# Kernel tuning notes

Hardware: AMD Instinct MI355X
Metric: run time of the kernel (lower is better)

The kernel has to match this reference:

```python
import jax, jax.numpy as jnp
import numpy as np

N, E, T = 10000, 160000, 1600000
D, C, H = 256, 64, 1024  # d_model, d_message/channels, 4*d_model ffn hidden


def setup_inputs() -> dict:
    key = jax.random.key(0)
    ks = jax.random.split(key, 20)
    rn = lambda k, s, sc=1.0: jax.random.normal(k, s, dtype=jnp.float32) * sc
    return {
        "x": rn(ks[0], (N, D)),
        "y": rn(ks[1], (E, D)),
        "r": rn(ks[2], (E, 3)),
        "src": jax.random.randint(ks[3], (E,), 0, N),
        "dst": jax.random.randint(ks[4], (E,), 0, N),
        "tsrc": jax.random.randint(ks[5], (T,), 0, E),
        "tdst": jax.random.randint(ks[6], (T,), 0, E),
        "W_src": rn(ks[7], (D, C), 0.05), "b_src": rn(ks[8], (C,), 0.05),
        "W_dst": rn(ks[9], (D, C), 0.05), "b_dst": rn(ks[10], (C,), 0.05),
        "W_edge": rn(ks[11], (D, C), 0.05), "b_edge": rn(ks[12], (C,), 0.05),
        "attn": rn(ks[13], (C,), 0.05),
        "W1": rn(ks[14], (C, H), 0.05), "b1": rn(ks[15], (H,), 0.05),
        "W2": rn(ks[16], (H, D), 0.05), "b2": rn(ks[17], (D,), 0.05),
    }


def reference(x, y, r, src, dst, tsrc, tdst,
              W_src, b_src, W_dst, b_dst, W_edge, b_edge,
              attn, W1, b1, W2, b2):
    # per-bond message: xij = Lin_src(x)[src] + Lin_dst(x)[dst] + Lin_edge(y)  -> (E, C)
    xij = (x @ W_src + b_src)[src] + (x @ W_dst + b_dst)[dst] + (y @ W_edge + b_edge)

    # triplet angle cosine via normalized (negated) bond vectors  -> (T,)
    rnorm = -r / jnp.linalg.norm(r, axis=1, keepdims=True)
    cos_jik = jnp.clip(jnp.sum(rnorm[tsrc] * rnorm[tdst], axis=-1), -1.0 + 1e-6, 1.0 - 1e-6)

    # Chebyshev expansion: T_n(cos) = cos(n * arccos(cos))  -> (T, C)
    n = jnp.arange(C, dtype=jnp.float32)
    z_jik = jnp.cos(n[None, :] * jnp.arccos(cos_jik)[:, None])

    # triplet feature and attention logit
    e_jik = jax.nn.silu(z_jik + xij[tsrc] + xij[tdst])          # (T, C)
    logits = e_jik @ attn                                        # (T,)

    # segment softmax over triplets grouped by destination bond (edge_softmax)
    mx = jax.ops.segment_max(logits, tdst, num_segments=E)
    ex = jnp.exp(logits - mx[tdst])
    den = jax.ops.segment_sum(ex, tdst, num_segments=E)
    a = ex / den[tdst]                                           # (T,)

    # attention-weighted scatter-sum of neighbor bond features  -> (E, C)
    ft = jax.ops.segment_sum(xij[tsrc] * a[:, None], tdst, num_segments=E)

    # feedforward: Linear -> SiLU -> Linear  -> (E, D)
    return jax.nn.silu(ft @ W1 + b1) @ W2 + b2
```

## Files before the change

kernel.cpp:

```cpp
#include <hip/hip_runtime.h>

#define N_NODES 10000
#define N_EDGES 160000
#define N_TRI   1600000
#define DM      256
#define CH      64
#define HH      1024
#define ECHUNK  40000

typedef short bf16x8 __attribute__((ext_vector_type(8)));
typedef float f32x4  __attribute__((ext_vector_type(4)));

__device__ __forceinline__ unsigned short f2bf(float f) {
  unsigned int u = __float_as_uint(f);
  u += 0x7fff + ((u >> 16) & 1);
  return (unsigned short)(u >> 16);
}

__global__ __launch_bounds__(256) void k_node_proj(
    const float* __restrict__ x, const float* __restrict__ Ws, const float* __restrict__ bs,
    const float* __restrict__ Wd, const float* __restrict__ bd,
    float* __restrict__ xs, float* __restrict__ xd) {
  __shared__ float xl[4][DM];
  int tid = threadIdx.x;
  int n0 = blockIdx.x * 4;
  for (int i = tid; i < 4 * DM; i += 256) xl[i >> 8][i & 255] = x[n0 * DM + i];
  __syncthreads();
  int c = tid & 63, g = tid >> 6;
  float as = bs[c], ad = bd[c];
  for (int d = 0; d < DM; d++) {
    float xv = xl[g][d];
    as += xv * Ws[d * CH + c];
    ad += xv * Wd[d * CH + c];
  }
  int n = n0 + g;
  xs[n * CH + c] = as;
  xd[n * CH + c] = ad;
}

__global__ __launch_bounds__(256) void k_edge_proj(
    const float* __restrict__ y, const float* __restrict__ We, const float* __restrict__ be,
    const float* __restrict__ xs, const float* __restrict__ xd,
    const int* __restrict__ src, const int* __restrict__ dst,
    float* __restrict__ xij) {
  __shared__ float yl[16][DM];
  int tid = threadIdx.x;
  int e0 = blockIdx.x * 16;
  for (int i = tid; i < 16 * DM; i += 256) yl[i >> 8][i & 255] = y[e0 * DM + i];
  __syncthreads();
  int c = tid & 63, g = tid >> 6;
  float acc[4];
#pragma unroll
  for (int s = 0; s < 4; s++) acc[s] = be[c];
  for (int d = 0; d < DM; d += 4) {
    float w0 = We[(d + 0) * CH + c];
    float w1 = We[(d + 1) * CH + c];
    float w2 = We[(d + 2) * CH + c];
    float w3 = We[(d + 3) * CH + c];
#pragma unroll
    for (int s = 0; s < 4; s++) {
      const float4 yv = *(const float4*)&yl[g * 4 + s][d];
      acc[s] += yv.x * w0 + yv.y * w1 + yv.z * w2 + yv.w * w3;
    }
  }
#pragma unroll
  for (int s = 0; s < 4; s++) {
    int e = e0 + g * 4 + s;
    xij[e * CH + c] = acc[s] + xs[src[e] * CH + c] + xd[dst[e] * CH + c];
  }
}

__global__ void k_rnorm(const float* __restrict__ r, float4* __restrict__ rn4) {
  int e = blockIdx.x * 256 + threadIdx.x;
  if (e >= N_EDGES) return;
  float a = r[e * 3 + 0], b = r[e * 3 + 1], c = r[e * 3 + 2];
  float inv = rsqrtf(a * a + b * b + c * c);
  rn4[e] = (float4){-a * inv, -b * inv, -c * inv, 0.f};
}

__global__ __launch_bounds__(256) void k_theta(
    const float4* __restrict__ rn4, const int* __restrict__ tsrc, const int* __restrict__ tdst,
    float* __restrict__ theta) {
  int t = blockIdx.x * 256 + threadIdx.x;
  if (t >= N_TRI) return;
  float4 a = rn4[tsrc[t]];
  float4 b = rn4[tdst[t]];
  float c = a.x * b.x + a.y * b.y + a.z * b.z;
  c = fminf(fmaxf(c, -1.0f + 1e-6f), 1.0f - 1e-6f);
  theta[t] = acosf(c);
}

__global__ void k_hist(const int* __restrict__ tdst, int* __restrict__ cnt) {
  int t = blockIdx.x * 256 + threadIdx.x;
  if (t < N_TRI) atomicAdd(&cnt[tdst[t]], 1);
}

__global__ __launch_bounds__(256) void k_scan_sum(const int* __restrict__ cnt,
                                                  int* __restrict__ bsum, int n) {
  __shared__ int s[256];
  int b = blockIdx.x, tid = threadIdx.x;
  int tot = 0;
#pragma unroll
  for (int i = 0; i < 8; i++) {
    int idx = b * 2048 + i * 256 + tid;
    if (idx < n) tot += cnt[idx];
  }
  s[tid] = tot;
  __syncthreads();
  for (int off = 128; off > 0; off >>= 1) {
    if (tid < off) s[tid] += s[tid + off];
    __syncthreads();
  }
  if (tid == 0) bsum[b] = s[0];
}

__global__ void k_scan_top(int* __restrict__ bsum, int nb, int* __restrict__ start_last) {
  if (threadIdx.x == 0) {
    int run = 0;
    for (int i = 0; i < nb; i++) {
      int v = bsum[i];
      bsum[i] = run;
      run += v;
    }
    *start_last = run;
  }
}

__global__ __launch_bounds__(256) void k_scan_apply(const int* __restrict__ cnt,
                                                    const int* __restrict__ bsum,
                                                    int* __restrict__ start,
                                                    int* __restrict__ cur, int n) {
  __shared__ int s[256];
  int b = blockIdx.x, tid = threadIdx.x;
  int base = b * 2048 + tid * 8;
  int loc[8];
  int tot = 0;
#pragma unroll
  for (int i = 0; i < 8; i++) {
    int idx = base + i;
    int v = (idx < n) ? cnt[idx] : 0;
    loc[i] = tot;
    tot += v;
  }
  s[tid] = tot;
  __syncthreads();
  for (int off = 1; off < 256; off <<= 1) {
    int t2 = 0;
    if (tid >= off) t2 = s[tid - off];
    __syncthreads();
    if (tid >= off) s[tid] += t2;
    __syncthreads();
  }
  int excl = s[tid] - tot + bsum[b];
#pragma unroll
  for (int i = 0; i < 8; i++) {
    int idx = base + i;
    if (idx < n) {
      int v = excl + loc[i];
      start[idx] = v;
      cur[idx] = v;
    }
  }
}

__global__ void k_scatter(const int* __restrict__ tdst, int* __restrict__ cur,
                          int* __restrict__ sorted) {
  int t = blockIdx.x * 256 + threadIdx.x;
  if (t < N_TRI) {
    int p = atomicAdd(&cur[tdst[t]], 1);
    sorted[p] = t;
  }
}

__global__ __launch_bounds__(256) void k_attn_ft(
    const int* __restrict__ start, const int* __restrict__ sorted,
    const float* __restrict__ theta, const int* __restrict__ tsrc,
    const float* __restrict__ xij, const float* __restrict__ attn,
    unsigned short* __restrict__ ft) {
  int tid = threadIdx.x;
  int e = blockIdx.x * 4 + (tid >> 6);
  int lane = tid & 63;
  float lanef = (float)lane;
  int beg = start[e], end = start[e + 1];
  int deg = end - beg;
  float xd = xij[e * CH + lane];
  float av = attn[lane];
  float m = -1e30f, den = 0.f, acc = 0.f;
  if (deg > 0 && deg <= 64) {
    int ts_ = 0;
    float th_ = 0.f;
    if (lane < deg) {
      int t = sorted[beg + lane];
      ts_ = tsrc[t];
      th_ = theta[t];
    }
    int ts_cur = __shfl(ts_, 0);
    float th_cur = __shfl(th_, 0);
    float xs_cur = xij[ts_cur * CH + lane];
    for (int i = 0; i < deg; i++) {
      float th_nxt = 0.f, xs_nxt = 0.f;
      if (i + 1 < deg) {
        int ts_nxt = __shfl(ts_, i + 1);
        th_nxt = __shfl(th_, i + 1);
        xs_nxt = xij[ts_nxt * CH + lane];
      }
      float v = __cosf(th_cur * lanef) + xs_cur + xd;
      float sv = v / (1.0f + __expf(-v));
      float contrib = sv * av;
#pragma unroll
      for (int off = 32; off; off >>= 1) contrib += __shfl_xor(contrib, off);
      float mn = fmaxf(m, contrib);
      float scale = __expf(m - mn);
      float p = __expf(contrib - mn);
      den = den * scale + p;
      acc = acc * scale + p * xs_cur;
      m = mn;
      th_cur = th_nxt;
      xs_cur = xs_nxt;
    }
  } else if (deg > 64) {
    for (int i = 0; i < deg; i++) {
      int t = sorted[beg + i];
      int ts = tsrc[t];
      float th = theta[t];
      float xs = xij[ts * CH + lane];
      float v = __cosf(th * lanef) + xs + xd;
      float sv = v / (1.0f + __expf(-v));
      float contrib = sv * av;
#pragma unroll
      for (int off = 32; off; off >>= 1) contrib += __shfl_xor(contrib, off);
      float mn = fmaxf(m, contrib);
      float scale = __expf(m - mn);
      float p = __expf(contrib - mn);
      den = den * scale + p;
      acc = acc * scale + p * xs;
      m = mn;
    }
  }
  ft[e * CH + lane] = f2bf(deg > 0 ? acc / den : 0.f);
}

__global__ __launch_bounds__(256) void k_prep_w1p(const float* __restrict__ W1,
                                                  unsigned short* __restrict__ W1P) {
  int idx = blockIdx.x * 256 + threadIdx.x;
  int k = idx & 63, row = idx >> 6;
  int i = row & 15, t = (row >> 4) & 1, hb = row >> 5;
  int hidden = hb * 32 + ((i >> 2) << 3) + (t << 2) + (i & 3);
  W1P[idx] = f2bf(W1[k * HH + hidden]);
}

__global__ __launch_bounds__(256) void k_prep_w2t(const float* __restrict__ W2,
                                                  unsigned short* __restrict__ W2T) {
  int idx = blockIdx.x * 256 + threadIdx.x;
  int n = idx >> 10, k = idx & 1023;
  W2T[idx] = f2bf(W2[k * DM + n]);
}

__global__ __launch_bounds__(256) void k_ffn_g1(
    const unsigned short* __restrict__ ft, const unsigned short* __restrict__ W1P,
    const float* __restrict__ b1, unsigned short* __restrict__ hpk) {
  int tid = threadIdx.x;
  int w = tid >> 6, lane = tid & 63;
  int l16 = lane & 15, q = lane >> 4;
  int tile = blockIdx.x;
  int e0 = tile * 64;

  bf16x8 ftf[4][2];
#pragma unroll
  for (int mt = 0; mt < 4; mt++)
#pragma unroll
    for (int s = 0; s < 2; s++)
      ftf[mt][s] = *(const bf16x8*)&ft[(size_t)(e0 + mt * 16 + l16) * CH + s * 32 + q * 8];

#pragma unroll
  for (int hbl = 0; hbl < 2; hbl++) {
    int hb = blockIdx.y * 8 + w * 2 + hbl;
    bf16x8 w1f[2][2];
#pragma unroll
    for (int t = 0; t < 2; t++)
#pragma unroll
      for (int s = 0; s < 2; s++)
        w1f[t][s] = *(const bf16x8*)&W1P[(size_t)((hb * 2 + t) * 16 + l16) * 64 + s * 32 + q * 8];
    const float4 bv0 = *(const float4*)&b1[hb * 32 + q * 8];
    const float4 bv1 = *(const float4*)&b1[hb * 32 + q * 8 + 4];
#pragma unroll
    for (int mt = 0; mt < 4; mt++) {
      f32x4 h0 = (f32x4){0.f, 0.f, 0.f, 0.f};
      f32x4 h1 = (f32x4){0.f, 0.f, 0.f, 0.f};
      h0 = __builtin_amdgcn_mfma_f32_16x16x32_bf16(w1f[0][0], ftf[mt][0], h0, 0, 0, 0);
      h0 = __builtin_amdgcn_mfma_f32_16x16x32_bf16(w1f[0][1], ftf[mt][1], h0, 0, 0, 0);
      h1 = __builtin_amdgcn_mfma_f32_16x16x32_bf16(w1f[1][0], ftf[mt][0], h1, 0, 0, 0);
      h1 = __builtin_amdgcn_mfma_f32_16x16x32_bf16(w1f[1][1], ftf[mt][1], h1, 0, 0, 0);
      float v0 = h0[0] + bv0.x, v1 = h0[1] + bv0.y, v2 = h0[2] + bv0.z, v3 = h0[3] + bv0.w;
      float u0 = h1[0] + bv1.x, u1 = h1[1] + bv1.y, u2 = h1[2] + bv1.z, u3 = h1[3] + bv1.w;
      float s0 = v0 / (1.f + __expf(-v0)), s1 = v1 / (1.f + __expf(-v1));
      float s2 = v2 / (1.f + __expf(-v2)), s3 = v3 / (1.f + __expf(-v3));
      float t0 = u0 / (1.f + __expf(-u0)), t1 = u1 / (1.f + __expf(-u1));
      float t2 = u2 / (1.f + __expf(-u2)), t3 = u3 / (1.f + __expf(-u3));
      union { bf16x8 v; unsigned int u[4]; } pa;
      pa.u[0] = ((unsigned int)f2bf(s1) << 16) | f2bf(s0);
      pa.u[1] = ((unsigned int)f2bf(s3) << 16) | f2bf(s2);
      pa.u[2] = ((unsigned int)f2bf(t1) << 16) | f2bf(t0);
      pa.u[3] = ((unsigned int)f2bf(t3) << 16) | f2bf(t2);
      *(bf16x8*)&hpk[((((size_t)tile * 32 + hb) * 4 + mt) * 64 + lane) * 8] = pa.v;
    }
  }
}

__global__ __launch_bounds__(128) void k_ffn_g2(
    const unsigned short* __restrict__ hpk, const unsigned short* __restrict__ W2T,
    const float* __restrict__ b2, float* __restrict__ out) {
  int tid = threadIdx.x;
  int w = tid >> 6, lane = tid & 63;
  int l16 = lane & 15, q = lane >> 4;
  int tile = blockIdx.x >> 1;
  int ch = blockIdx.x & 1;
  int colBase = ch * 128 + w * 64;
  int e0 = tile * 64;

  f32x4 acc[4][4];
#pragma unroll
  for (int mt = 0; mt < 4; mt++)
#pragma unroll
    for (int nt = 0; nt < 4; nt++) acc[mt][nt] = (f32x4){0.f, 0.f, 0.f, 0.f};

  for (int hb = 0; hb < 32; hb++) {
    bf16x8 pam[4], bw[4];
#pragma unroll
    for (int mt = 0; mt < 4; mt++)
      pam[mt] = *(const bf16x8*)&hpk[((((size_t)tile * 32 + hb) * 4 + mt) * 64 + lane) * 8];
#pragma unroll
    for (int nt = 0; nt < 4; nt++)
      bw[nt] = *(const bf16x8*)&W2T[(size_t)(colBase + nt * 16 + l16) * HH + hb * 32 + q * 8];
#pragma unroll
    for (int nt = 0; nt < 4; nt++)
#pragma unroll
      for (int mt = 0; mt < 4; mt++)
        acc[mt][nt] = __builtin_amdgcn_mfma_f32_16x16x32_bf16(pam[mt], bw[nt], acc[mt][nt], 0, 0, 0);
  }

#pragma unroll
  for (int nt = 0; nt < 4; nt++) {
    int col = colBase + nt * 16 + l16;
    float b2v = b2[col];
#pragma unroll
    for (int mt = 0; mt < 4; mt++) {
      int erow = e0 + mt * 16 + q * 4;
#pragma unroll
      for (int r = 0; r < 4; r++)
        out[(size_t)(erow + r) * DM + col] = acc[mt][nt][r] + b2v;
    }
  }
}

extern "C" void kernel_launch(void* const* d_in, const int* in_sizes, int n_in,
                              void* d_out, int out_size, void* d_ws, size_t ws_size,
                              hipStream_t stream) {
  (void)in_sizes; (void)n_in; (void)out_size; (void)ws_size;
  const float* x      = (const float*)d_in[0];
  const float* y      = (const float*)d_in[1];
  const float* r      = (const float*)d_in[2];
  const int*   src    = (const int*)d_in[3];
  const int*   dst    = (const int*)d_in[4];
  const int*   tsrc   = (const int*)d_in[5];
  const int*   tdst   = (const int*)d_in[6];
  const float* W_src  = (const float*)d_in[7];
  const float* b_src  = (const float*)d_in[8];
  const float* W_dst  = (const float*)d_in[9];
  const float* b_dst  = (const float*)d_in[10];
  const float* W_edge = (const float*)d_in[11];
  const float* b_edge = (const float*)d_in[12];
  const float* attn   = (const float*)d_in[13];
  const float* W1     = (const float*)d_in[14];
  const float* b1     = (const float*)d_in[15];
  const float* W2     = (const float*)d_in[16];
  const float* b2     = (const float*)d_in[17];
  float* out = (float*)d_out;

  char* wsp = (char*)d_ws;
  auto alloc = [&](size_t bytes) -> char* {
    char* p = wsp;
    wsp += (bytes + 255) & ~(size_t)255;
    return p;
  };
  float* xs     = (float*)alloc((size_t)N_NODES * CH * 4);
  float* xd     = (float*)alloc((size_t)N_NODES * CH * 4);
  float* xij    = (float*)alloc((size_t)N_EDGES * CH * 4);
  float4* rn4   = (float4*)alloc((size_t)N_EDGES * 16);
  float* theta  = (float*)alloc((size_t)N_TRI * 4);
  int*   cnt    = (int*)alloc((size_t)N_EDGES * 4);
  int*   start  = (int*)alloc((size_t)(N_EDGES + 1) * 4);
  int*   cur    = (int*)alloc((size_t)N_EDGES * 4);
  int*   bsum   = (int*)alloc(1024 * 4);
  int*   sorted = (int*)alloc((size_t)N_TRI * 4);
  unsigned short* ftb = (unsigned short*)alloc((size_t)N_EDGES * CH * 2);
  unsigned short* W1P = (unsigned short*)alloc((size_t)CH * HH * 2);
  unsigned short* W2T = (unsigned short*)alloc((size_t)HH * DM * 2);
  unsigned short* hpk = (unsigned short*)alloc((size_t)ECHUNK * HH * 2);

  const int NB = (N_EDGES + 2047) / 2048;

  k_prep_w1p<<<(CH * HH) / 256, 256, 0, stream>>>(W1, W1P);
  k_prep_w2t<<<(HH * DM) / 256, 256, 0, stream>>>(W2, W2T);

  k_node_proj<<<N_NODES / 4, 256, 0, stream>>>(x, W_src, b_src, W_dst, b_dst, xs, xd);
  k_rnorm<<<N_EDGES / 256, 256, 0, stream>>>(r, rn4);
  k_edge_proj<<<N_EDGES / 16, 256, 0, stream>>>(y, W_edge, b_edge, xs, xd, src, dst, xij);
  k_theta<<<N_TRI / 256, 256, 0, stream>>>(rn4, tsrc, tdst, theta);

  hipMemsetAsync(cnt, 0, (size_t)N_EDGES * 4, stream);
  k_hist<<<N_TRI / 256, 256, 0, stream>>>(tdst, cnt);
  k_scan_sum<<<NB, 256, 0, stream>>>(cnt, bsum, N_EDGES);
  k_scan_top<<<1, 64, 0, stream>>>(bsum, NB, &start[N_EDGES]);
  k_scan_apply<<<NB, 256, 0, stream>>>(cnt, bsum, start, cur, N_EDGES);
  k_scatter<<<N_TRI / 256, 256, 0, stream>>>(tdst, cur, sorted);

  k_attn_ft<<<N_EDGES / 4, 256, 0, stream>>>(start, sorted, theta, tsrc, xij, attn, ftb);

  const int TILES = ECHUNK / 64;
  for (int c = 0; c < N_EDGES / ECHUNK; c++) {
    const size_t E0 = (size_t)c * ECHUNK;
    k_ffn_g1<<<dim3(TILES, 4), 256, 0, stream>>>(ftb + E0 * CH, W1P, b1, hpk);
    k_ffn_g2<<<TILES * 2, 128, 0, stream>>>(hpk, W2T, b2, out + E0 * DM);
  }
}
```

Measured before the change: 1.260 ms.

## Compute edge projection with split-bf16 MFMA and widen FFN second GEMM blocks

Replaces the scalar fp32 edge projection (y @ W_edge) with a matrix-core kernel. Both y and W_edge are split into high and low bf16 parts, and three MFMA products are summed to approximate fp32 accuracy. A prep kernel writes the transposed split weights. Separately, k_ffn_g2 now uses 256-thread blocks with four waves covering all 256 output columns, where before it used two blocks of 128 threads per tile. This cuts block count and improves reuse of the A fragments. Dropping the lo*lo term costs a little precision.

```diff
diff --git a/kernel.cpp b/kernel.cpp
--- a/kernel.cpp
+++ b/kernel.cpp
@@ -38,35 +38,74 @@
   xd[n * CH + c] = ad;
 }
 
-__global__ __launch_bounds__(256) void k_edge_proj(
-    const float* __restrict__ y, const float* __restrict__ We, const float* __restrict__ be,
+__global__ __launch_bounds__(256) void k_prep_wehl(const float* __restrict__ We,
+                                                   unsigned short* __restrict__ WehT,
+                                                   unsigned short* __restrict__ WelT) {
+  int idx = blockIdx.x * 256 + threadIdx.x;
+  int c = idx >> 8, d = idx & 255;
+  float wv = We[d * CH + c];
+  unsigned int b = __float_as_uint(wv);
+  float whf = __uint_as_float(b & 0xffff0000u);
+  float wl = wv - whf;
+  WehT[idx] = (unsigned short)(b >> 16);
+  WelT[idx] = (unsigned short)(__float_as_uint(wl) >> 16);
+}
+
+__global__ __launch_bounds__(256) void k_edge_mfma(
+    const float* __restrict__ y, const unsigned short* __restrict__ WehT,
+    const unsigned short* __restrict__ WelT, const float* __restrict__ be,
     const float* __restrict__ xs, const float* __restrict__ xd,
     const int* __restrict__ src, const int* __restrict__ dst,
     float* __restrict__ xij) {
-  __shared__ float yl[16][DM];
   int tid = threadIdx.x;
-  int e0 = blockIdx.x * 16;
-  for (int i = tid; i < 16 * DM; i += 256) yl[i >> 8][i & 255] = y[e0 * DM + i];
-  __syncthreads();
-  int c = tid & 63, g = tid >> 6;
-  float acc[4];
-#pragma unroll
-  for (int s = 0; s < 4; s++) acc[s] = be[c];
-  for (int d = 0; d < DM; d += 4) {
-    float w0 = We[(d + 0) * CH + c];
-    float w1 = We[(d + 1) * CH + c];
-    float w2 = We[(d + 2) * CH + c];
-    float w3 = We[(d + 3) * CH + c];
-#pragma unroll
-    for (int s = 0; s < 4; s++) {
-      const float4 yv = *(const float4*)&yl[g * 4 + s][d];
-      acc[s] += yv.x * w0 + yv.y * w1 + yv.z * w2 + yv.w * w3;
-    }
-  }
-#pragma unroll
-  for (int s = 0; s < 4; s++) {
-    int e = e0 + g * 4 + s;
-    xij[e * CH + c] = acc[s] + xs[src[e] * CH + c] + xd[dst[e] * CH + c];
+  int w = tid >> 6, lane = tid & 63;
+  int l16 = lane & 15, q = lane >> 4;
+  int e0 = blockIdx.x * 64;
+  int arow = e0 + w * 16 + l16;
+
+  f32x4 acc[4];
+#pragma unroll
+  for (int nt = 0; nt < 4; nt++) acc[nt] = (f32x4){0.f, 0.f, 0.f, 0.f};
+
+  for (int s = 0; s < 8; s++) {
+    const float4* yp = (const float4*)&y[(size_t)arow * DM + s * 32 + q * 8];
+    float4 ya = yp[0], yb = yp[1];
+    float el[8] = {ya.x, ya.y, ya.z, ya.w, yb.x, yb.y, yb.z, yb.w};
+    union { bf16x8 v; unsigned int u[4]; } ah, al;
+#pragma unroll
+    for (int j = 0; j < 4; j++) {
+      unsigned int b0 = __float_as_uint(el[2 * j]);
+      unsigned int b1 = __float_as_uint(el[2 * j + 1]);
+      ah.u[j] = (b0 >> 16) | (b1 & 0xffff0000u);
+      float h0 = __uint_as_float(b0 & 0xffff0000u);
+      float h1 = __uint_as_float(b1 & 0xffff0000u);
+      unsigned int l0 = __float_as_uint(el[2 * j] - h0);
+      unsigned int l1 = __float_as_uint(el[2 * j + 1] - h1);
+      al.u[j] = (l0 >> 16) | (l1 & 0xffff0000u);
+    }
+#pragma unroll
+    for (int nt = 0; nt < 4; nt++) {
+      bf16x8 bh = *(const bf16x8*)&WehT[(nt * 16 + l16) * DM + s * 32 + q * 8];
+      bf16x8 bl = *(const bf16x8*)&WelT[(nt * 16 + l16) * DM + s * 32 + q * 8];
+      acc[nt] = __builtin_amdgcn_mfma_f32_16x16x32_bf16(ah.v, bh, acc[nt], 0, 0, 0);
+      acc[nt] = __builtin_amdgcn_mfma_f32_16x16x32_bf16(al.v, bh, acc[nt], 0, 0, 0);
+      acc[nt] = __builtin_amdgcn_mfma_f32_16x16x32_bf16(ah.v, bl, acc[nt], 0, 0, 0);
+    }
+  }
+
+  int er = e0 + w * 16 + q * 4;
+  int sv[4], dv[4];
+#pragma unroll
+  for (int r = 0; r < 4; r++) { sv[r] = src[er + r]; dv[r] = dst[er + r]; }
+#pragma unroll
+  for (int nt = 0; nt < 4; nt++) {
+    int col = nt * 16 + l16;
+    float bev = be[col];
+#pragma unroll
+    for (int r = 0; r < 4; r++) {
+      float v = acc[nt][r] + bev + xs[sv[r] * CH + col] + xd[dv[r] * CH + col];
+      xij[(size_t)(er + r) * CH + col] = v;
+    }
   }
 }
 
@@ -307,15 +346,14 @@
   }
 }
 
-__global__ __launch_bounds__(128) void k_ffn_g2(
+__global__ __launch_bounds__(256) void k_ffn_g2(
     const unsigned short* __restrict__ hpk, const unsigned short* __restrict__ W2T,
     const float* __restrict__ b2, float* __restrict__ out) {
   int tid = threadIdx.x;
   int w = tid >> 6, lane = tid & 63;
   int l16 = lane & 15, q = lane >> 4;
-  int tile = blockIdx.x >> 1;
-  int ch = blockIdx.x & 1;
-  int colBase = ch * 128 + w * 64;
+  int tile = blockIdx.x;
+  int colBase = w * 64;
   int e0 = tile * 64;
 
   f32x4 acc[4][4];
@@ -393,19 +431,22 @@
   int*   cur    = (int*)alloc((size_t)N_EDGES * 4);
   int*   bsum   = (int*)alloc(1024 * 4);
   int*   sorted = (int*)alloc((size_t)N_TRI * 4);
-  unsigned short* ftb = (unsigned short*)alloc((size_t)N_EDGES * CH * 2);
-  unsigned short* W1P = (unsigned short*)alloc((size_t)CH * HH * 2);
-  unsigned short* W2T = (unsigned short*)alloc((size_t)HH * DM * 2);
-  unsigned short* hpk = (unsigned short*)alloc((size_t)ECHUNK * HH * 2);
+  unsigned short* ftb  = (unsigned short*)alloc((size_t)N_EDGES * CH * 2);
+  unsigned short* W1P  = (unsigned short*)alloc((size_t)CH * HH * 2);
+  unsigned short* W2T  = (unsigned short*)alloc((size_t)HH * DM * 2);
+  unsigned short* WehT = (unsigned short*)alloc((size_t)CH * DM * 2);
+  unsigned short* WelT = (unsigned short*)alloc((size_t)CH * DM * 2);
+  unsigned short* hpk  = (unsigned short*)alloc((size_t)ECHUNK * HH * 2);
 
   const int NB = (N_EDGES + 2047) / 2048;
 
   k_prep_w1p<<<(CH * HH) / 256, 256, 0, stream>>>(W1, W1P);
   k_prep_w2t<<<(HH * DM) / 256, 256, 0, stream>>>(W2, W2T);
+  k_prep_wehl<<<(CH * DM) / 256, 256, 0, stream>>>(W_edge, WehT, WelT);
 
   k_node_proj<<<N_NODES / 4, 256, 0, stream>>>(x, W_src, b_src, W_dst, b_dst, xs, xd);
   k_rnorm<<<N_EDGES / 256, 256, 0, stream>>>(r, rn4);
-  k_edge_proj<<<N_EDGES / 16, 256, 0, stream>>>(y, W_edge, b_edge, xs, xd, src, dst, xij);
+  k_edge_mfma<<<N_EDGES / 64, 256, 0, stream>>>(y, WehT, WelT, b_edge, xs, xd, src, dst, xij);
   k_theta<<<N_TRI / 256, 256, 0, stream>>>(rn4, tsrc, tdst, theta);
 
   hipMemsetAsync(cnt, 0, (size_t)N_EDGES * 4, stream);
@@ -421,6 +462,6 @@
   for (int c = 0; c < N_EDGES / ECHUNK; c++) {
     const size_t E0 = (size_t)c * ECHUNK;
     k_ffn_g1<<<dim3(TILES, 4), 256, 0, stream>>>(ftb + E0 * CH, W1P, b1, hpk);
-    k_ffn_g2<<<TILES * 2, 128, 0, stream>>>(hpk, W2T, b2, out + E0 * DM);
-  }
-}
+    k_ffn_g2<<<TILES, 256, 0, stream>>>(hpk, W2T, b2, out + E0 * DM);
+  }
+}
```

New measurement: 1.282 ms. Within noise of the previous version (+1.8%).
